# Kernel optimization log

Measured on AMD Instinct MI355X. Metric: run time of the kernel, lower is better.

## Reference

```python
import jax, jax.numpy as jnp
import numpy as np

EPS_BN = 1e-5
EPS_RENORM = 1e-9

def conv_bn_relu(x, W, g, b, m, v):
    # x: [B, Cin, N], W: [Cout, Cin] (1x1 conv, no bias). Eval-mode BN.
    y = jnp.einsum('oi,bin->bon', W, x)
    scale = (g / jnp.sqrt(v + EPS_BN))[None, :, None]
    bias = (b - m * g / jnp.sqrt(v + EPS_BN))[None, :, None]
    return jax.nn.relu(y * scale + bias)

def _make_params(key, cout, cin):
    k1, k2, k3, k4 = jax.random.split(key, 4)
    W = jax.random.normal(k1, (cout, cin), jnp.float32) * (1.0 / np.sqrt(cin))
    g = jax.random.uniform(k2, (cout,), jnp.float32, 0.5, 1.5)
    b = jax.random.normal(k3, (cout,), jnp.float32) * 0.1
    m = jax.random.normal(k4, (cout,), jnp.float32) * 0.1
    v = jax.random.uniform(jax.random.fold_in(key, 7), (cout,), jnp.float32, 0.5, 1.5)
    return W, g, b, m, v

def setup_inputs() -> dict:
    key = jax.random.key(0)
    ks = jax.random.split(key, 6)
    B, C, N = 8, 1024, 2048
    x = jax.random.normal(ks[0], (B, C, N), jnp.float32)
    inp = {'x': x}
    dims = [(1024, 1024), (1024, 1024), (128, 1024), (128, 1024), (1024, 1024)]
    for i, (co, ci) in enumerate(dims):
        W, g, b, m, v = _make_params(ks[i + 1], co, ci)
        inp[f'W{i+1}'] = W
        inp[f'g{i+1}'] = g
        inp[f'b{i+1}'] = b
        inp[f'm{i+1}'] = m
        inp[f'v{i+1}'] = v
    return inp

def reference(x,
              W1, g1, b1, m1, v1,
              W2, g2, b2, m2, v2,
              W3, g3, b3, m3, v3,
              W4, g4, b4, m4, v4,
              W5, g5, b5, m5, v5):
    x1 = conv_bn_relu(x, W1, g1, b1, m1, v1)          # [B,1024,N]
    v_ = conv_bn_relu(x1, W2, g2, b2, m2, v2)         # [B,1024,N]
    q_ = conv_bn_relu(x1, W3, g3, b3, m3, v3)         # [B,128,N]
    k_ = conv_bn_relu(x1, W4, g4, b4, m4, v4)         # [B,128,N]
    # q transposed: [B,N,128] @ [B,128,N] -> [B,N,N]
    scores = jnp.einsum('bcn,bcm->bnm', q_, k_)
    scores = jax.nn.softmax(scores, axis=-1)
    scores = scores / (EPS_RENORM + scores.sum(axis=1, keepdims=True))
    attn = jnp.einsum('bcn,bnm->bcm', v_, scores)     # [B,1024,N]
    x2 = conv_bn_relu(x1 - attn, W5, g5, b5, m5, v5)
    return x1 + x2
```

## Files before the change

### kernel.cpp

```cpp
#include <hip/hip_runtime.h>

typedef unsigned short u16;
using bf16x8 = __attribute__((ext_vector_type(8))) short;
using f32x4  = __attribute__((ext_vector_type(4))) float;

#define CH   1024
#define NP   2048
#define CQ   128

__device__ __forceinline__ float bf2f(u16 u){
  union { unsigned u; float f; } c; c.u = ((unsigned)u) << 16; return c.f;
}
__device__ __forceinline__ u16 f2bf(float f){
  unsigned x = __float_as_uint(f);
  unsigned r = (x + 0x7fffu + ((x >> 16) & 1u)) >> 16;
  return (u16)r;
}

__device__ __forceinline__ void gl2lds16(const u16* g, u16* l){
  __builtin_amdgcn_global_load_lds(
      (const __attribute__((address_space(1))) unsigned int*)(const void*)g,
      (__attribute__((address_space(3))) unsigned int*)(void*)l,
      16, 0, 0);
}

__global__ void ws_marker(float* out, float have_mb){
  out[0] = 1048576.0f + have_mb;
}

__global__ __launch_bounds__(256) void transpose_split(const float* __restrict__ x,
                                                       u16* __restrict__ xh,
                                                       u16* __restrict__ xl){
  const int bb = blockIdx.z;
  const int n0 = blockIdx.x * 64, c0 = blockIdx.y * 64;
  __shared__ float tile[64][65];
  const int t = threadIdx.x;
  const float* xb = x + ((size_t)bb*CH + c0)*NP + n0;
#pragma unroll
  for (int rr = 0; rr < 4; ++rr){
    const int c_l = (t >> 4) + rr*16;
    const int n_l = (t & 15) * 4;
    float4 v = *(const float4*)&xb[(size_t)c_l*NP + n_l];
    tile[c_l][n_l+0] = v.x; tile[c_l][n_l+1] = v.y;
    tile[c_l][n_l+2] = v.z; tile[c_l][n_l+3] = v.w;
  }
  __syncthreads();
  u16* oh = xh + ((size_t)bb*NP + n0)*CH + c0;
  u16* ol = xl + ((size_t)bb*NP + n0)*CH + c0;
#pragma unroll
  for (int rr = 0; rr < 4; ++rr){
    const int n_l = (t >> 4) + rr*16;
    const int c_l = (t & 15) * 4;
    ushort4 h, l;
    float v0 = tile[c_l+0][n_l], v1 = tile[c_l+1][n_l];
    float v2 = tile[c_l+2][n_l], v3 = tile[c_l+3][n_l];
    h.x = f2bf(v0); l.x = f2bf(v0 - bf2f(h.x));
    h.y = f2bf(v1); l.y = f2bf(v1 - bf2f(h.y));
    h.z = f2bf(v2); l.z = f2bf(v2 - bf2f(h.z));
    h.w = f2bf(v3); l.w = f2bf(v3 - bf2f(h.w));
    *(ushort4*)&oh[(size_t)n_l*CH + c_l] = h;
    *(ushort4*)&ol[(size_t)n_l*CH + c_l] = l;
  }
}

__global__ __launch_bounds__(256) void prep_all(
    const float* __restrict__ w0, const float* __restrict__ w1,
    const float* __restrict__ w2, const float* __restrict__ w3,
    const float* __restrict__ w4,
    u16* w1h, u16* w1l, u16* w2h,
    u16* w34h, u16* w34l, u16* w5h,
    const float* g3, const float* b3, const float* m3, const float* v3,
    const float* g4, const float* b4, const float* m4, const float* v4,
    float* p34, float* colsum){
  const int seg = blockIdx.y;
  if (seg == 5){
    for (int i = blockIdx.x*blockDim.x + threadIdx.x; i < 1024; i += gridDim.x*blockDim.x){
      const int grp = i >> 8, j = i & 255;
      const float* pa = (grp==0) ? g3 : (grp==1) ? b3 : (grp==2) ? m3 : v3;
      const float* pb = (grp==0) ? g4 : (grp==1) ? b4 : (grp==2) ? m4 : v4;
      p34[i] = (j < 128) ? pa[j] : pb[j-128];
    }
    return;
  }
  if (seg == 6){
    for (int i = blockIdx.x*blockDim.x + threadIdx.x; i < 8*NP; i += gridDim.x*blockDim.x)
      colsum[i] = 0.f;
    return;
  }
  const float* w; u16 *wh, *wl; int n;
  switch (seg){
    case 0:  w = w0; wh = w1h;           wl = w1l;           n = CH*CH; break;
    case 1:  w = w1; wh = w2h;           wl = nullptr;       n = CH*CH; break;
    case 2:  w = w2; wh = w34h;          wl = w34l;          n = CQ*CH; break;
    case 3:  w = w3; wh = w34h + CQ*CH;  wl = w34l + CQ*CH;  n = CQ*CH; break;
    default: w = w4; wh = w5h;           wl = nullptr;       n = CH*CH; break;
  }
  for (int i = blockIdx.x*blockDim.x + threadIdx.x; i < n; i += gridDim.x*blockDim.x){
    float v = w[i];
    u16 h = f2bf(v);
    wh[i] = h;
    if (wl) wl[i] = f2bf(v - bf2f(h));
  }
}

template<int EPI>
__global__ __launch_bounds__(256, 4) void gemm_plain(
    const u16* __restrict__ A, const u16* __restrict__ B,
    int lda, int ldb, long astr, long bstr, int K,
    void* __restrict__ out0, long ostr, int ldo,
    const float* __restrict__ pg, const float* __restrict__ pb,
    const float* __restrict__ pm, const float* __restrict__ pv,
    const u16* __restrict__ x1h, const u16* __restrict__ x1l,
    const float* __restrict__ cinv, const u16* __restrict__ cbf)
{
  __shared__ __align__(16) u16 sA[8192], sB[8192];
  const int tid  = threadIdx.x;
  const int lane = tid & 63, wave = tid >> 6;
  const int wr = wave & 1, wc = wave >> 1;
  const int l15 = lane & 15, q = lane >> 4;
  const int id = blockIdx.x;
  const int bb = id & 7;
  const int rest = id >> 3;
  const int by = rest & 7;
  const int bx = rest >> 3;
  const u16* Ab = A + (size_t)bb*astr + (size_t)bx*128*lda;
  const u16* Bb = B + (size_t)bb*bstr + (size_t)by*128*ldb;

  f32x4 acc[4][4] = {};
  f32x4 accR[4] = {};

  const int srow = tid >> 3;
  const int schunk = tid & 7;

  for (int kt = 0; kt < K; kt += 64){
#pragma unroll
    for (int r = 0; r < 4; ++r){
      const int row = r*32 + srow;
      const int gc8 = ((schunk ^ (row & 7)) << 3);
      gl2lds16(Ab + (size_t)row*lda + kt + gc8, &sA[r*2048 + tid*8]);
      gl2lds16(Bb + (size_t)row*ldb + kt + gc8, &sB[r*2048 + tid*8]);
    }
    __syncthreads();
#pragma unroll
    for (int s = 0; s < 2; ++s){
      bf16x8 af[4], bfr[4];
#pragma unroll
      for (int i = 0; i < 4; ++i){
        const int ra = wr*64 + i*16 + l15;
        af[i]  = *(const bf16x8*)&sA[ra*64 + (((s*4 + q) ^ (ra & 7)) << 3)];
        const int rb = wc*64 + i*16 + l15;
        bfr[i] = *(const bf16x8*)&sB[rb*64 + (((s*4 + q) ^ (rb & 7)) << 3)];
      }
      if constexpr (EPI == 1){
        const bf16x8 bcs = *(const bf16x8*)&cbf[(size_t)bb*NP + kt + s*32 + q*8];
#pragma unroll
        for (int i = 0; i < 4; ++i)
          accR[i] = __builtin_amdgcn_mfma_f32_16x16x32_bf16(af[i], bcs, accR[i], 0, 0, 0);
      }
#pragma unroll
      for (int i = 0; i < 4; ++i)
#pragma unroll
        for (int j = 0; j < 4; ++j)
          acc[i][j] = __builtin_amdgcn_mfma_f32_16x16x32_bf16(af[i], bfr[j], acc[i][j], 0, 0, 0);
    }
    __syncthreads();
  }

  const int rbase = bx*128 + wr*64;
  const int cbase = by*128 + wc*64;
#pragma unroll
  for (int j = 0; j < 4; ++j){
    const int gc = cbase + j*16 + l15;
    float scale = 0.f, bias = 0.f;
    if (EPI == 0 || EPI == 2){
      scale = pg[gc] * rsqrtf(pv[gc] + 1e-5f);
      bias  = pb[gc] - pm[gc]*scale;
    }
#pragma unroll
    for (int i = 0; i < 4; ++i){
      const int gr0 = rbase + i*16 + q*4;
      if (EPI == 0){
        const float4 cv = *(const float4*)&cinv[(size_t)bb*NP + gr0];
        ushort4 pk;
        pk.x = f2bf(fmaxf(acc[i][j][0]*scale + bias, 0.f) * cv.x);
        pk.y = f2bf(fmaxf(acc[i][j][1]*scale + bias, 0.f) * cv.y);
        pk.z = f2bf(fmaxf(acc[i][j][2]*scale + bias, 0.f) * cv.z);
        pk.w = f2bf(fmaxf(acc[i][j][3]*scale + bias, 0.f) * cv.w);
        *(ushort4*)&((u16*)out0)[(size_t)bb*ostr + (size_t)gc*ldo + gr0] = pk;
      } else if (EPI == 1){
#pragma unroll
        for (int r = 0; r < 4; ++r){
          const int gr = gr0 + r;
          const size_t idx = (size_t)bb*ostr + (size_t)gr*ldo + gc;
          const float rsv = 1.f / (1e-9f + accR[i][r]);
          const float x1v = bf2f(x1h[idx]) + bf2f(x1l[idx]);
          ((u16*)out0)[idx] = f2bf(x1v - acc[i][j][r]*rsv);
        }
      } else {
        float4 o4;
#pragma unroll
        for (int r = 0; r < 4; ++r){
          const int gr = gr0 + r;
          const size_t xidx = (size_t)bb*((size_t)NP*CH) + (size_t)gr*CH + gc;
          const float x2  = fmaxf(acc[i][j][r]*scale + bias, 0.f);
          const float x1v = bf2f(x1h[xidx]) + bf2f(x1l[xidx]);
          (&o4.x)[r] = x1v + x2;
        }
        *(float4*)&((float*)out0)[(size_t)bb*ostr + (size_t)gc*ldo + gr0] = o4;
      }
    }
  }
}

template<int EPI>
__global__ __launch_bounds__(256, 4) void gemm_split3(
    const u16* __restrict__ Ah, const u16* __restrict__ Al,
    const u16* __restrict__ Bh, const u16* __restrict__ Bl,
    int lda, int ldb, long astr, long bstr, int K,
    u16* __restrict__ outH, u16* __restrict__ outL,
    long ostr, int ldo,
    const float* __restrict__ pg, const float* __restrict__ pb,
    const float* __restrict__ pm, const float* __restrict__ pv,
    float* __restrict__ colsum, int gymask, int gyshift)
{
  __shared__ __align__(16) u16 sAh[4096], sAl[4096], sBh[4096], sBl[4096];
  const int tid  = threadIdx.x;
  const int lane = tid & 63, wave = tid >> 6;
  const int wr = wave & 1, wc = wave >> 1;
  const int l15 = lane & 15, q = lane >> 4;
  const int id = blockIdx.x;
  const int bb = id & 7;
  const int rest = id >> 3;
  const int by = rest & gymask;
  const int bx = rest >> gyshift;
  const u16* Abh = Ah + (size_t)bb*astr + (size_t)bx*128*lda;
  const u16* Abl = Al + (size_t)bb*astr + (size_t)bx*128*lda;
  const u16* Bbh = Bh + (size_t)bb*bstr + (size_t)by*128*ldb;
  const u16* Bbl = Bl + (size_t)bb*bstr + (size_t)by*128*ldb;

  f32x4 acc[4][4] = {};

  const int r0 = tid >> 2, r1 = r0 + 64;
  const int cs = (((tid & 3) ^ ((r0 >> 1) & 3)) << 3);

  int offA[4], offB[4];
#pragma unroll
  for (int i = 0; i < 4; ++i){
    const int ra = wr*64 + i*16 + l15;
    offA[i] = ra*32 + ((q ^ ((ra >> 1) & 3)) << 3);
    const int rb = wc*64 + i*16 + l15;
    offB[i] = rb*32 + ((q ^ ((rb >> 1) & 3)) << 3);
  }

  for (int kt = 0; kt < K; kt += 32){
    gl2lds16(Abh + (size_t)r0*lda + kt + cs, &sAh[tid*8]);
    gl2lds16(Abh + (size_t)r1*lda + kt + cs, &sAh[2048 + tid*8]);
    gl2lds16(Abl + (size_t)r0*lda + kt + cs, &sAl[tid*8]);
    gl2lds16(Abl + (size_t)r1*lda + kt + cs, &sAl[2048 + tid*8]);
    gl2lds16(Bbh + (size_t)r0*ldb + kt + cs, &sBh[tid*8]);
    gl2lds16(Bbh + (size_t)r1*ldb + kt + cs, &sBh[2048 + tid*8]);
    gl2lds16(Bbl + (size_t)r0*ldb + kt + cs, &sBl[tid*8]);
    gl2lds16(Bbl + (size_t)r1*ldb + kt + cs, &sBl[2048 + tid*8]);
    __syncthreads();
    bf16x8 ah[4], al[4], bh2[4], bl2[4];
#pragma unroll
    for (int i = 0; i < 4; ++i){
      ah[i] = *(const bf16x8*)&sAh[offA[i]];
      al[i] = *(const bf16x8*)&sAl[offA[i]];
    }
#pragma unroll
    for (int j = 0; j < 4; ++j){
      bh2[j] = *(const bf16x8*)&sBh[offB[j]];
      bl2[j] = *(const bf16x8*)&sBl[offB[j]];
    }
#pragma unroll
    for (int i = 0; i < 4; ++i)
#pragma unroll
      for (int j = 0; j < 4; ++j){
        acc[i][j] = __builtin_amdgcn_mfma_f32_16x16x32_bf16(ah[i], bh2[j], acc[i][j], 0, 0, 0);
        acc[i][j] = __builtin_amdgcn_mfma_f32_16x16x32_bf16(ah[i], bl2[j], acc[i][j], 0, 0, 0);
        acc[i][j] = __builtin_amdgcn_mfma_f32_16x16x32_bf16(al[i], bh2[j], acc[i][j], 0, 0, 0);
      }
    __syncthreads();
  }

  const int rbase = bx*128 + wr*64;
  const int cbase = by*128 + wc*64;

  if constexpr (EPI == 1){
    __shared__ float colpart[128];
    if (tid < 128) colpart[tid] = 0.f;
    __syncthreads();
#pragma unroll
    for (int j = 0; j < 4; ++j){
      const int gc = cbase + j*16 + l15;
      float lsum = 0.f;
#pragma unroll
      for (int i = 0; i < 4; ++i){
        const int gr0 = rbase + i*16 + q*4;
#pragma unroll
        for (int r = 0; r < 4; ++r){
          const float e = __expf(fminf(acc[i][j][r], 85.f));
          outH[(size_t)bb*ostr + (size_t)(gr0 + r)*ldo + gc] = f2bf(e);
          lsum += e;
        }
      }
      atomicAdd(&colpart[wc*64 + j*16 + l15], lsum);
    }
    __syncthreads();
    if (tid < 128) atomicAdd(&colsum[(size_t)bb*NP + (size_t)by*128 + tid], colpart[tid]);
  } else {
#pragma unroll
    for (int j = 0; j < 4; ++j){
      const int gc = cbase + j*16 + l15;
      const float scale = pg[gc] * rsqrtf(pv[gc] + 1e-5f);
      const float bias  = pb[gc] - pm[gc]*scale;
#pragma unroll
      for (int i = 0; i < 4; ++i){
        const int gr0 = rbase + i*16 + q*4;
#pragma unroll
        for (int r = 0; r < 4; ++r){
          const size_t idx = (size_t)bb*ostr + (size_t)(gr0 + r)*ldo + gc;
          const float y = fmaxf(acc[i][j][r]*scale + bias, 0.f);
          const u16 h = f2bf(y);
          outH[idx] = h;
          outL[idx] = f2bf(y - bf2f(h));
        }
      }
    }
  }
}

__global__ __launch_bounds__(256) void colinv_k(const float* __restrict__ cs,
                                                float* __restrict__ ci,
                                                u16* __restrict__ cib, int n){
  const int i = blockIdx.x*blockDim.x + threadIdx.x;
  if (i < n){
    const float v = 1.0f / cs[i];
    ci[i]  = v;
    cib[i] = f2bf(v);
  }
}

extern "C" void kernel_launch(void* const* d_in, const int* in_sizes, int n_in,
                              void* d_out, int out_size, void* d_ws, size_t ws_size,
                              hipStream_t stream){
  const float* x = (const float*)d_in[0];
  const float *W[5], *g[5], *bt[5], *mu[5], *vr[5];
  for (int i = 0; i < 5; ++i){
    W[i]  = (const float*)d_in[1 + 5*i + 0];
    g[i]  = (const float*)d_in[1 + 5*i + 1];
    bt[i] = (const float*)d_in[1 + 5*i + 2];
    mu[i] = (const float*)d_in[1 + 5*i + 3];
    vr[i] = (const float*)d_in[1 + 5*i + 4];
  }

  char* wp = (char*)d_ws;
  size_t off = 0;
  auto take = [&](size_t bytes) -> void* {
    void* p = wp + off;
    off = (off + bytes + 255) & ~(size_t)255;
    return p;
  };
  u16*   xh   = (u16*)take(33554432);
  u16*   xl   = (u16*)take(33554432);
  u16*   x1h  = (u16*)take(33554432);
  u16*   x1l  = (u16*)take(33554432);
  u16*   qkh  = (u16*)take(8388608);
  u16*   qkl  = (u16*)take(8388608);
  float* csum = (float*)take(65536);
  float* cinv = (float*)take(65536);
  u16*   cibf = (u16*)take(32768);
  u16*   w1h  = (u16*)take(2097152);
  u16*   w1l  = (u16*)take(2097152);
  u16*   w2h  = (u16*)take(2097152);
  u16*   w34h = (u16*)take(524288);
  u16*   w34l = (u16*)take(524288);
  u16*   w5h  = (u16*)take(2097152);
  float* p34  = (float*)take(4096);

  if (ws_size < off){
    ws_marker<<<1, 1, 0, stream>>>((float*)d_out, (float)(ws_size >> 20));
    return;
  }

  u16* vh   = xh;
  u16* tt   = xl;
  u16* expS = (u16*)d_out;

  prep_all<<<dim3(256, 7), 256, 0, stream>>>(
      W[0], W[1], W[2], W[3], W[4],
      w1h, w1l, w2h, w34h, w34l, w5h,
      g[2], bt[2], mu[2], vr[2], g[3], bt[3], mu[3], vr[3],
      p34, csum);

  transpose_split<<<dim3(32,16,8), 256, 0, stream>>>(x, xh, xl);

  gemm_split3<0><<<dim3(1024), 256, 0, stream>>>(
      xh, xl, w1h, w1l, CH, CH, (long)NP*CH, 0, CH,
      x1h, x1l, (long)NP*CH, CH, g[0], bt[0], mu[0], vr[0], nullptr, 7, 3);

  gemm_split3<0><<<dim3(256), 256, 0, stream>>>(
      x1h, x1l, w34h, w34l, CH, CH, (long)NP*CH, 0, CH,
      qkh, qkl, (long)NP*256, 256, p34, p34+256, p34+512, p34+768, nullptr, 1, 1);

  gemm_split3<1><<<dim3(2048), 256, 0, stream>>>(
      qkh + 128, qkl + 128, qkh, qkl, 256, 256, (long)NP*256, (long)NP*256, CQ,
      expS, nullptr, (long)NP*NP, NP,
      nullptr, nullptr, nullptr, nullptr, csum, 15, 4);

  colinv_k<<<dim3(64), 256, 0, stream>>>(csum, cinv, cibf, 8*NP);

  gemm_plain<0><<<dim3(1024), 256, 0, stream>>>(
      x1h, w2h, CH, CH, (long)NP*CH, 0, CH,
      vh, (long)CH*NP, NP, g[1], bt[1], mu[1], vr[1],
      nullptr, nullptr, cinv, nullptr);

  gemm_plain<1><<<dim3(1024), 256, 0, stream>>>(
      expS, vh, NP, NP, (long)NP*NP, (long)CH*NP, NP,
      tt, (long)NP*CH, CH, nullptr, nullptr, nullptr, nullptr,
      x1h, x1l, nullptr, cibf);

  gemm_plain<2><<<dim3(1024), 256, 0, stream>>>(
      tt, w5h, CH, CH, (long)NP*CH, 0, CH,
      d_out, (long)CH*NP, NP, g[4], bt[4], mu[4], vr[4],
      x1h, x1l, nullptr, nullptr);
}
```

Measured before the change: 645.4 us.

## Replace plain GEMM with 256x256-tile, 4-stage async-pipelined deep GEMM

The bf16 GEMM kernel used for the V projection, the attention-times-V product and the final conv now uses 512-thread blocks. Each block computes a 256x256 output tile with a K-step of 32 and a 4-deep ring of LDS buffers. Loads go directly from global memory to LDS three stages ahead, gated by explicit vmcnt waits and a single barrier per step, so loads overlap with MFMA work. For the attention GEMM, the column-inverse vector is cached in LDS. The cost is a large LDS footprint (about 132KB), more accumulator registers, and only 256 blocks, which may leave some of the mi355x's 256 CUs underfilled or limit occupancy to one block per CU.

```diff
diff --git a/kernel.cpp b/kernel.cpp
--- a/kernel.cpp
+++ b/kernel.cpp
@@ -104,7 +104,7 @@
 }
 
 template<int EPI>
-__global__ __launch_bounds__(256, 4) void gemm_plain(
+__global__ __launch_bounds__(512, 2) void gemm_deep(
     const u16* __restrict__ A, const u16* __restrict__ B,
     int lda, int ldb, long astr, long bstr, int K,
     void* __restrict__ out0, long ostr, int ldo,
@@ -113,61 +113,99 @@
     const u16* __restrict__ x1h, const u16* __restrict__ x1l,
     const float* __restrict__ cinv, const u16* __restrict__ cbf)
 {
-  __shared__ __align__(16) u16 sA[8192], sB[8192];
+  __shared__ __align__(16) u16 sA[4*8192];
+  __shared__ __align__(16) u16 sB[4*8192];
+  __shared__ __align__(16) u16 cl[2048];
+
   const int tid  = threadIdx.x;
-  const int lane = tid & 63, wave = tid >> 6;
-  const int wr = wave & 1, wc = wave >> 1;
+  const int lane = tid & 63;
+  const int wave = tid >> 6;
+  const int wr = wave >> 2, wc = wave & 3;
   const int l15 = lane & 15, q = lane >> 4;
   const int id = blockIdx.x;
   const int bb = id & 7;
   const int rest = id >> 3;
-  const int by = rest & 7;
-  const int bx = rest >> 3;
-  const u16* Ab = A + (size_t)bb*astr + (size_t)bx*128*lda;
-  const u16* Bb = B + (size_t)bb*bstr + (size_t)by*128*ldb;
-
-  f32x4 acc[4][4] = {};
-  f32x4 accR[4] = {};
-
-  const int srow = tid >> 3;
-  const int schunk = tid & 7;
-
-  for (int kt = 0; kt < K; kt += 64){
-#pragma unroll
-    for (int r = 0; r < 4; ++r){
-      const int row = r*32 + srow;
-      const int gc8 = ((schunk ^ (row & 7)) << 3);
-      gl2lds16(Ab + (size_t)row*lda + kt + gc8, &sA[r*2048 + tid*8]);
-      gl2lds16(Bb + (size_t)row*ldb + kt + gc8, &sB[r*2048 + tid*8]);
-    }
+  const int by = rest & 3;
+  const int bx = rest >> 2;
+
+  const u16* Ab = A + (size_t)bb*astr + (size_t)bx*256*lda;
+  const u16* Bb = B + (size_t)bb*bstr + (size_t)by*256*ldb;
+
+  const int srow = tid >> 2;
+  const int schunk = tid & 3;
+  const int cA = ((schunk ^ ((srow >> 1) & 3)) << 3);
+
+  auto stage = [&](int t){
+    const int buf = (t & 3) << 13;
+    const int kt = t << 5;
+    gl2lds16(Ab + (size_t)srow*lda + kt + cA,           &sA[buf + tid*8]);
+    gl2lds16(Ab + (size_t)(srow + 128)*lda + kt + cA,   &sA[buf + 4096 + tid*8]);
+    gl2lds16(Bb + (size_t)srow*ldb + kt + cA,           &sB[buf + tid*8]);
+    gl2lds16(Bb + (size_t)(srow + 128)*ldb + kt + cA,   &sB[buf + 4096 + tid*8]);
+  };
+
+  int offA[8], offB[4];
+#pragma unroll
+  for (int i = 0; i < 8; ++i){
+    const int ra = wr*128 + i*16 + l15;
+    offA[i] = ra*32 + ((q ^ ((ra >> 1) & 3)) << 3);
+  }
+#pragma unroll
+  for (int j = 0; j < 4; ++j){
+    const int rb = wc*64 + j*16 + l15;
+    offB[j] = rb*32 + ((q ^ ((rb >> 1) & 3)) << 3);
+  }
+
+  if constexpr (EPI == 1){
+    if (tid < 256)
+      *(bf16x8*)&cl[tid*8] = *(const bf16x8*)&cbf[(size_t)bb*NP + tid*8];
     __syncthreads();
-#pragma unroll
-    for (int s = 0; s < 2; ++s){
-      bf16x8 af[4], bfr[4];
-#pragma unroll
-      for (int i = 0; i < 4; ++i){
-        const int ra = wr*64 + i*16 + l15;
-        af[i]  = *(const bf16x8*)&sA[ra*64 + (((s*4 + q) ^ (ra & 7)) << 3)];
-        const int rb = wc*64 + i*16 + l15;
-        bfr[i] = *(const bf16x8*)&sB[rb*64 + (((s*4 + q) ^ (rb & 7)) << 3)];
-      }
-      if constexpr (EPI == 1){
-        const bf16x8 bcs = *(const bf16x8*)&cbf[(size_t)bb*NP + kt + s*32 + q*8];
-#pragma unroll
-        for (int i = 0; i < 4; ++i)
-          accR[i] = __builtin_amdgcn_mfma_f32_16x16x32_bf16(af[i], bcs, accR[i], 0, 0, 0);
-      }
-#pragma unroll
-      for (int i = 0; i < 4; ++i)
+  }
+
+  f32x4 acc[8][4] = {};
+  f32x4 accR[8] = {};
+
+  const int NT = K >> 5;
+  stage(0);
+  if (NT > 1) stage(1);
+  if (NT > 2) stage(2);
+
+  for (int t = 0; t < NT; ++t){
+    if (t < NT - 2)       asm volatile("s_waitcnt vmcnt(8)" ::: "memory");
+    else if (t == NT - 2) asm volatile("s_waitcnt vmcnt(4)" ::: "memory");
+    else                  asm volatile("s_waitcnt vmcnt(0)" ::: "memory");
+    __builtin_amdgcn_s_barrier();
+    asm volatile("" ::: "memory");
+    if (t + 3 < NT) stage(t + 3);
+
+    const int buf = (t & 3) << 13;
+    bf16x8 bv[4];
+#pragma unroll
+    for (int j = 0; j < 4; ++j) bv[j] = *(const bf16x8*)&sB[buf + offB[j]];
+
+    if constexpr (EPI == 1){
+      const bf16x8 cbs = *(const bf16x8*)&cl[(t << 5) + q*8];
+#pragma unroll
+      for (int i = 0; i < 8; ++i){
+        const bf16x8 a = *(const bf16x8*)&sA[buf + offA[i]];
+        accR[i] = __builtin_amdgcn_mfma_f32_16x16x32_bf16(a, cbs, accR[i], 0, 0, 0);
 #pragma unroll
         for (int j = 0; j < 4; ++j)
-          acc[i][j] = __builtin_amdgcn_mfma_f32_16x16x32_bf16(af[i], bfr[j], acc[i][j], 0, 0, 0);
-    }
-    __syncthreads();
-  }
-
-  const int rbase = bx*128 + wr*64;
-  const int cbase = by*128 + wc*64;
+          acc[i][j] = __builtin_amdgcn_mfma_f32_16x16x32_bf16(a, bv[j], acc[i][j], 0, 0, 0);
+      }
+    } else {
+#pragma unroll
+      for (int i = 0; i < 8; ++i){
+        const bf16x8 a = *(const bf16x8*)&sA[buf + offA[i]];
+#pragma unroll
+        for (int j = 0; j < 4; ++j)
+          acc[i][j] = __builtin_amdgcn_mfma_f32_16x16x32_bf16(a, bv[j], acc[i][j], 0, 0, 0);
+      }
+    }
+  }
+
+  const int rbase = bx*256 + wr*128;
+  const int cbase = by*256 + wc*64;
 #pragma unroll
   for (int j = 0; j < 4; ++j){
     const int gc = cbase + j*16 + l15;
@@ -177,7 +215,7 @@
       bias  = pb[gc] - pm[gc]*scale;
     }
 #pragma unroll
-    for (int i = 0; i < 4; ++i){
+    for (int i = 0; i < 8; ++i){
       const int gr0 = rbase + i*16 + q*4;
       if (EPI == 0){
         const float4 cv = *(const float4*)&cinv[(size_t)bb*NP + gr0];
@@ -411,17 +449,17 @@
 
   colinv_k<<<dim3(64), 256, 0, stream>>>(csum, cinv, cibf, 8*NP);
 
-  gemm_plain<0><<<dim3(1024), 256, 0, stream>>>(
+  gemm_deep<0><<<dim3(256), 512, 0, stream>>>(
       x1h, w2h, CH, CH, (long)NP*CH, 0, CH,
       vh, (long)CH*NP, NP, g[1], bt[1], mu[1], vr[1],
       nullptr, nullptr, cinv, nullptr);
 
-  gemm_plain<1><<<dim3(1024), 256, 0, stream>>>(
+  gemm_deep<1><<<dim3(256), 512, 0, stream>>>(
       expS, vh, NP, NP, (long)NP*NP, (long)CH*NP, NP,
       tt, (long)NP*CH, CH, nullptr, nullptr, nullptr, nullptr,
       x1h, x1l, nullptr, cibf);
 
-  gemm_plain<2><<<dim3(1024), 256, 0, stream>>>(
+  gemm_deep<2><<<dim3(256), 512, 0, stream>>>(
       tt, w5h, CH, CH, (long)NP*CH, 0, CH,
       d_out, (long)CH*NP, NP, g[4], bt[4], mu[4], vr[4],
       x1h, x1l, nullptr, nullptr);
```

Result: slower. 707.1 us (+9.6%).

## Replace plain bf16 GEMMs with 256x256-tile 8-wave ping-pong pipelined kernel

Applied to the files above, without the earlier changes.

Rewrites the three single-precision-input GEMMs (V projection, attention apply, final conv) into a 512-thread kernel with 256x256 output tiles. It double-buffers LDS and issues async global-to-LDS loads for the next K-step interleaved across four MFMA phases, using s_setprio and explicit barriers. The goal is to hide global latency and cut redundant A/B reloads through larger tiles. The cost is larger LDS use (about 132KB), lower occupancy, and a grid of only 256 blocks, which may underfill the CUs.

```diff
diff --git a/kernel.cpp b/kernel.cpp
--- a/kernel.cpp
+++ b/kernel.cpp
@@ -104,7 +104,7 @@
 }
 
 template<int EPI>
-__global__ __launch_bounds__(256, 4) void gemm_plain(
+__global__ __launch_bounds__(512, 2) void gemm_8p(
     const u16* __restrict__ A, const u16* __restrict__ B,
     int lda, int ldb, long astr, long bstr, int K,
     void* __restrict__ out0, long ostr, int ldo,
@@ -113,63 +113,152 @@
     const u16* __restrict__ x1h, const u16* __restrict__ x1l,
     const float* __restrict__ cinv, const u16* __restrict__ cbf)
 {
-  __shared__ __align__(16) u16 sA[8192], sB[8192];
+  __shared__ __align__(16) u16 sA[4*8192];
+  __shared__ __align__(16) u16 sB[4*8192];
+  __shared__ __align__(16) u16 cl[2048];
+
   const int tid  = threadIdx.x;
-  const int lane = tid & 63, wave = tid >> 6;
-  const int wr = wave & 1, wc = wave >> 1;
+  const int lane = tid & 63;
+  const int wave = tid >> 6;
+  const int wr = wave >> 1, wc = wave & 1;
   const int l15 = lane & 15, q = lane >> 4;
   const int id = blockIdx.x;
   const int bb = id & 7;
   const int rest = id >> 3;
-  const int by = rest & 7;
-  const int bx = rest >> 3;
-  const u16* Ab = A + (size_t)bb*astr + (size_t)bx*128*lda;
-  const u16* Bb = B + (size_t)bb*bstr + (size_t)by*128*ldb;
-
-  f32x4 acc[4][4] = {};
+  const int by = rest & 3;
+  const int bx = rest >> 2;
+
+  const u16* Ab = A + (size_t)bb*astr + (size_t)bx*256*lda;
+  const u16* Bb = B + (size_t)bb*bstr + (size_t)by*256*ldb;
+
+  const int sr0 = tid >> 3;
+  const int sg  = ((tid & 7) ^ (sr0 & 7)) << 3;
+
+  auto stageA = [&](int half, int V){
+    u16* dst = &sA[((((V & 1) << 1) + half) << 13)];
+    const u16* src = Ab + (size_t)(half*128 + sr0)*lda + V*64 + sg;
+    gl2lds16(src, dst + tid*8);
+    gl2lds16(src + (size_t)64*lda, dst + 4096 + tid*8);
+  };
+  auto stageB = [&](int half, int V){
+    u16* dst = &sB[((((V & 1) << 1) + half) << 13)];
+    const u16* src = Bb + (size_t)(half*128 + sr0)*ldb + V*64 + sg;
+    gl2lds16(src, dst + tid*8);
+    gl2lds16(src + (size_t)64*ldb, dst + 4096 + tid*8);
+  };
+
+  const int ckx = l15 & 7;
+  const int ck0 = ((0 + q) ^ ckx) << 3;
+  const int ck1 = ((4 + q) ^ ckx) << 3;
+  int rpA[4], rpB[8];
+#pragma unroll
+  for (int i = 0; i < 4; ++i) rpA[i] = (((wr & 1) << 6) + i*16 + l15) << 6;
+#pragma unroll
+  for (int j = 0; j < 8; ++j) rpB[j] = (j*16 + l15) << 6;
+  const int aHalf = (wr >> 1) << 13;
+  const int bHalf = wc << 13;
+
+  if constexpr (EPI == 1){
+    if (tid < 256)
+      *(bf16x8*)&cl[tid*8] = *(const bf16x8*)&cbf[(size_t)bb*NP + tid*8];
+  }
+  __syncthreads();
+
+  f32x4 acc[4][8] = {};
   f32x4 accR[4] = {};
 
-  const int srow = tid >> 3;
-  const int schunk = tid & 7;
-
-  for (int kt = 0; kt < K; kt += 64){
-#pragma unroll
-    for (int r = 0; r < 4; ++r){
-      const int row = r*32 + srow;
-      const int gc8 = ((schunk ^ (row & 7)) << 3);
-      gl2lds16(Ab + (size_t)row*lda + kt + gc8, &sA[r*2048 + tid*8]);
-      gl2lds16(Bb + (size_t)row*ldb + kt + gc8, &sB[r*2048 + tid*8]);
-    }
-    __syncthreads();
-#pragma unroll
-    for (int s = 0; s < 2; ++s){
-      bf16x8 af[4], bfr[4];
-#pragma unroll
-      for (int i = 0; i < 4; ++i){
-        const int ra = wr*64 + i*16 + l15;
-        af[i]  = *(const bf16x8*)&sA[ra*64 + (((s*4 + q) ^ (ra & 7)) << 3)];
-        const int rb = wc*64 + i*16 + l15;
-        bfr[i] = *(const bf16x8*)&sB[rb*64 + (((s*4 + q) ^ (rb & 7)) << 3)];
-      }
-      if constexpr (EPI == 1){
-        const bf16x8 bcs = *(const bf16x8*)&cbf[(size_t)bb*NP + kt + s*32 + q*8];
-#pragma unroll
-        for (int i = 0; i < 4; ++i)
-          accR[i] = __builtin_amdgcn_mfma_f32_16x16x32_bf16(af[i], bcs, accR[i], 0, 0, 0);
-      }
+  const int NT = K >> 6;
+  stageA(0, 0); stageA(1, 0); stageB(0, 0); stageB(1, 0);
+  if (NT > 1) stageA(0, 1);
+
+  for (int U = 0; U < NT; ++U){
+    const int aB = ((U & 1) << 14) + aHalf;
+    const int bB = ((U & 1) << 14) + bHalf;
+    bf16x8 af[4], bfr[4], cbs;
+
+    if (U + 1 < NT) stageA(1, U + 1);
+    if (U < NT - 1) asm volatile("s_waitcnt vmcnt(4)" ::: "memory");
+    else            asm volatile("s_waitcnt vmcnt(0)" ::: "memory");
+    __builtin_amdgcn_s_barrier();
+#pragma unroll
+    for (int i = 0; i < 4; ++i) af[i]  = *(const bf16x8*)&sA[aB + rpA[i] + ck0];
+#pragma unroll
+    for (int j = 0; j < 4; ++j) bfr[j] = *(const bf16x8*)&sB[bB + rpB[j] + ck0];
+    if constexpr (EPI == 1) cbs = *(const bf16x8*)&cl[U*64 + q*8];
+    asm volatile("s_waitcnt lgkmcnt(0)" ::: "memory");
+    __builtin_amdgcn_sched_barrier(0);
+    __builtin_amdgcn_s_setprio(1);
+    if constexpr (EPI == 1){
 #pragma unroll
       for (int i = 0; i < 4; ++i)
-#pragma unroll
-        for (int j = 0; j < 4; ++j)
-          acc[i][j] = __builtin_amdgcn_mfma_f32_16x16x32_bf16(af[i], bfr[j], acc[i][j], 0, 0, 0);
-    }
-    __syncthreads();
-  }
-
-  const int rbase = bx*128 + wr*64;
-  const int cbase = by*128 + wc*64;
-#pragma unroll
-  for (int j = 0; j < 4; ++j){
+        accR[i] = __builtin_amdgcn_mfma_f32_16x16x32_bf16(af[i], cbs, accR[i], 0, 0, 0);
+    }
+#pragma unroll
+    for (int i = 0; i < 4; ++i)
+#pragma unroll
+      for (int j = 0; j < 4; ++j)
+        acc[i][j] = __builtin_amdgcn_mfma_f32_16x16x32_bf16(af[i], bfr[j], acc[i][j], 0, 0, 0);
+    __builtin_amdgcn_s_setprio(0);
+    __builtin_amdgcn_s_barrier();
+
+#pragma unroll
+    for (int j = 0; j < 4; ++j) bfr[j] = *(const bf16x8*)&sB[bB + rpB[4+j] + ck0];
+    if (U + 1 < NT) stageB(0, U + 1);
+    __builtin_amdgcn_s_barrier();
+    asm volatile("s_waitcnt lgkmcnt(0)" ::: "memory");
+    __builtin_amdgcn_sched_barrier(0);
+    __builtin_amdgcn_s_setprio(1);
+#pragma unroll
+    for (int i = 0; i < 4; ++i)
+#pragma unroll
+      for (int j = 0; j < 4; ++j)
+        acc[i][4+j] = __builtin_amdgcn_mfma_f32_16x16x32_bf16(af[i], bfr[j], acc[i][4+j], 0, 0, 0);
+    __builtin_amdgcn_s_setprio(0);
+    __builtin_amdgcn_s_barrier();
+
+#pragma unroll
+    for (int i = 0; i < 4; ++i) af[i]  = *(const bf16x8*)&sA[aB + rpA[i] + ck1];
+#pragma unroll
+    for (int j = 0; j < 4; ++j) bfr[j] = *(const bf16x8*)&sB[bB + rpB[j] + ck1];
+    if constexpr (EPI == 1) cbs = *(const bf16x8*)&cl[U*64 + 32 + q*8];
+    if (U + 1 < NT) stageB(1, U + 1);
+    __builtin_amdgcn_s_barrier();
+    asm volatile("s_waitcnt lgkmcnt(0)" ::: "memory");
+    __builtin_amdgcn_sched_barrier(0);
+    __builtin_amdgcn_s_setprio(1);
+    if constexpr (EPI == 1){
+#pragma unroll
+      for (int i = 0; i < 4; ++i)
+        accR[i] = __builtin_amdgcn_mfma_f32_16x16x32_bf16(af[i], cbs, accR[i], 0, 0, 0);
+    }
+#pragma unroll
+    for (int i = 0; i < 4; ++i)
+#pragma unroll
+      for (int j = 0; j < 4; ++j)
+        acc[i][j] = __builtin_amdgcn_mfma_f32_16x16x32_bf16(af[i], bfr[j], acc[i][j], 0, 0, 0);
+    __builtin_amdgcn_s_setprio(0);
+    __builtin_amdgcn_s_barrier();
+
+#pragma unroll
+    for (int j = 0; j < 4; ++j) bfr[j] = *(const bf16x8*)&sB[bB + rpB[4+j] + ck1];
+    if (U + 2 < NT) stageA(0, U + 2);
+    __builtin_amdgcn_s_barrier();
+    asm volatile("s_waitcnt lgkmcnt(0)" ::: "memory");
+    __builtin_amdgcn_sched_barrier(0);
+    __builtin_amdgcn_s_setprio(1);
+#pragma unroll
+    for (int i = 0; i < 4; ++i)
+#pragma unroll
+      for (int j = 0; j < 4; ++j)
+        acc[i][4+j] = __builtin_amdgcn_mfma_f32_16x16x32_bf16(af[i], bfr[j], acc[i][4+j], 0, 0, 0);
+    __builtin_amdgcn_s_setprio(0);
+    __builtin_amdgcn_s_barrier();
+  }
+
+  const int rbase = bx*256 + wr*64;
+  const int cbase = by*256 + wc*128;
+#pragma unroll
+  for (int j = 0; j < 8; ++j){
     const int gc = cbase + j*16 + l15;
     float scale = 0.f, bias = 0.f;
     if (EPI == 0 || EPI == 2){
@@ -411,17 +500,17 @@
 
   colinv_k<<<dim3(64), 256, 0, stream>>>(csum, cinv, cibf, 8*NP);
 
-  gemm_plain<0><<<dim3(1024), 256, 0, stream>>>(
+  gemm_8p<0><<<dim3(256), 512, 0, stream>>>(
       x1h, w2h, CH, CH, (long)NP*CH, 0, CH,
       vh, (long)CH*NP, NP, g[1], bt[1], mu[1], vr[1],
       nullptr, nullptr, cinv, nullptr);
 
-  gemm_plain<1><<<dim3(1024), 256, 0, stream>>>(
+  gemm_8p<1><<<dim3(256), 512, 0, stream>>>(
       expS, vh, NP, NP, (long)NP*NP, (long)CH*NP, NP,
       tt, (long)NP*CH, CH, nullptr, nullptr, nullptr, nullptr,
       x1h, x1l, nullptr, cibf);
 
-  gemm_plain<2><<<dim3(1024), 256, 0, stream>>>(
+  gemm_8p<2><<<dim3(256), 512, 0, stream>>>(
       tt, w5h, CH, CH, (long)NP*CH, 0, CH,
       d_out, (long)CH*NP, NP, g[4], bt[4], mu[4], vr[4],
       x1h, x1l, nullptr, nullptr);
```

Measured after the change: 628.8 us. 2.6% less time.

## Enlarge GEMM tiles to 256x256 with 512 threads and double-buffered LDS prefetch

Applied to the files above, without the earlier changes.

The plain bf16 GEMMs (V projection, attention apply and final conv) and the first split-precision conv GEMM move to 256x256 output tiles. Each uses 8 waves per block and a grid of 256 blocks. The next K-slice is loaded into a second LDS buffer while the current one is multiplied, and the column-scale vector for the attention GEMM is cached in LDS. This aims to cut global/LDS traffic per FLOP and hide load latency. In exchange it uses about 128KB of LDS per block, adds register pressure from 32 accumulators per wave, and runs at low occupancy with one block per CU.

```diff
diff --git a/kernel.cpp b/kernel.cpp
--- a/kernel.cpp
+++ b/kernel.cpp
@@ -104,7 +104,7 @@
 }
 
 template<int EPI>
-__global__ __launch_bounds__(256, 4) void gemm_plain(
+__global__ __launch_bounds__(512, 2) void gemm_2ph(
     const u16* __restrict__ A, const u16* __restrict__ B,
     int lda, int ldb, long astr, long bstr, int K,
     void* __restrict__ out0, long ostr, int ldo,
@@ -113,63 +113,99 @@
     const u16* __restrict__ x1h, const u16* __restrict__ x1l,
     const float* __restrict__ cinv, const u16* __restrict__ cbf)
 {
-  __shared__ __align__(16) u16 sA[8192], sB[8192];
+  __shared__ __align__(16) u16 sA[2][16384];
+  __shared__ __align__(16) u16 sB[2][16384];
+  __shared__ __align__(16) u16 cl[2048];
+
   const int tid  = threadIdx.x;
-  const int lane = tid & 63, wave = tid >> 6;
-  const int wr = wave & 1, wc = wave >> 1;
+  const int lane = tid & 63;
+  const int wave = tid >> 6;
+  const int wr = wave >> 1, wc = wave & 1;
   const int l15 = lane & 15, q = lane >> 4;
   const int id = blockIdx.x;
   const int bb = id & 7;
   const int rest = id >> 3;
-  const int by = rest & 7;
-  const int bx = rest >> 3;
-  const u16* Ab = A + (size_t)bb*astr + (size_t)bx*128*lda;
-  const u16* Bb = B + (size_t)bb*bstr + (size_t)by*128*ldb;
-
-  f32x4 acc[4][4] = {};
+  const int by = rest & 3;
+  const int bx = rest >> 2;
+
+  const u16* Ab = A + (size_t)bb*astr + (size_t)bx*256*lda;
+  const u16* Bb = B + (size_t)bb*bstr + (size_t)by*256*ldb;
+
+  const int sr0 = tid >> 3;
+  const int sg  = (((tid & 7) ^ (sr0 & 7)) << 3);
+
+  auto stage = [&](int kt, int bsel){
+    u16* dA = sA[bsel]; u16* dB = sB[bsel];
+#pragma unroll
+    for (int rr = 0; rr < 4; ++rr){
+      gl2lds16(Ab + (size_t)(rr*64 + sr0)*lda + kt + sg, dA + rr*4096 + tid*8);
+      gl2lds16(Bb + (size_t)(rr*64 + sr0)*ldb + kt + sg, dB + rr*4096 + tid*8);
+    }
+  };
+
+  int rpA[4], rpB[8];
+#pragma unroll
+  for (int i = 0; i < 4; ++i) rpA[i] = (wr*64 + i*16 + l15) << 6;
+#pragma unroll
+  for (int j = 0; j < 8; ++j) rpB[j] = (wc*128 + j*16 + l15) << 6;
+  const int ckx = l15 & 7;
+  const int ck0 = ((0 + q) ^ ckx) << 3;
+  const int ck1 = ((4 + q) ^ ckx) << 3;
+
+  if constexpr (EPI == 1){
+    if (tid < 256)
+      *(bf16x8*)&cl[tid*8] = *(const bf16x8*)&cbf[(size_t)bb*NP + tid*8];
+  }
+
+  f32x4 acc[4][8] = {};
   f32x4 accR[4] = {};
 
-  const int srow = tid >> 3;
-  const int schunk = tid & 7;
-
-  for (int kt = 0; kt < K; kt += 64){
-#pragma unroll
-    for (int r = 0; r < 4; ++r){
-      const int row = r*32 + srow;
-      const int gc8 = ((schunk ^ (row & 7)) << 3);
-      gl2lds16(Ab + (size_t)row*lda + kt + gc8, &sA[r*2048 + tid*8]);
-      gl2lds16(Bb + (size_t)row*ldb + kt + gc8, &sB[r*2048 + tid*8]);
-    }
+  const int NT = K >> 6;
+  stage(0, 0);
+  __syncthreads();
+
+  for (int t = 0; t < NT; ++t){
+    if (t + 1 < NT) stage((t + 1) << 6, (t + 1) & 1);
+    const u16* cA = sA[t & 1];
+    const u16* cB = sB[t & 1];
+    bf16x8 af[4], bfr[8];
+#pragma unroll
+    for (int i = 0; i < 4; ++i) af[i]  = *(const bf16x8*)&cA[rpA[i] + ck0];
+#pragma unroll
+    for (int j = 0; j < 8; ++j) bfr[j] = *(const bf16x8*)&cB[rpB[j] + ck0];
+    if constexpr (EPI == 1){
+      const bf16x8 cbs = *(const bf16x8*)&cl[(t << 6) + q*8];
+#pragma unroll
+      for (int i = 0; i < 4; ++i)
+        accR[i] = __builtin_amdgcn_mfma_f32_16x16x32_bf16(af[i], cbs, accR[i], 0, 0, 0);
+    }
+#pragma unroll
+    for (int i = 0; i < 4; ++i)
+#pragma unroll
+      for (int j = 0; j < 8; ++j)
+        acc[i][j] = __builtin_amdgcn_mfma_f32_16x16x32_bf16(af[i], bfr[j], acc[i][j], 0, 0, 0);
+#pragma unroll
+    for (int i = 0; i < 4; ++i) af[i]  = *(const bf16x8*)&cA[rpA[i] + ck1];
+#pragma unroll
+    for (int j = 0; j < 8; ++j) bfr[j] = *(const bf16x8*)&cB[rpB[j] + ck1];
+    if constexpr (EPI == 1){
+      const bf16x8 cbs = *(const bf16x8*)&cl[(t << 6) + 32 + q*8];
+#pragma unroll
+      for (int i = 0; i < 4; ++i)
+        accR[i] = __builtin_amdgcn_mfma_f32_16x16x32_bf16(af[i], cbs, accR[i], 0, 0, 0);
+    }
+#pragma unroll
+    for (int i = 0; i < 4; ++i)
+#pragma unroll
+      for (int j = 0; j < 8; ++j)
+        acc[i][j] = __builtin_amdgcn_mfma_f32_16x16x32_bf16(af[i], bfr[j], acc[i][j], 0, 0, 0);
     __syncthreads();
-#pragma unroll
-    for (int s = 0; s < 2; ++s){
-      bf16x8 af[4], bfr[4];
-#pragma unroll
-      for (int i = 0; i < 4; ++i){
-        const int ra = wr*64 + i*16 + l15;
-        af[i]  = *(const bf16x8*)&sA[ra*64 + (((s*4 + q) ^ (ra & 7)) << 3)];
-        const int rb = wc*64 + i*16 + l15;
-        bfr[i] = *(const bf16x8*)&sB[rb*64 + (((s*4 + q) ^ (rb & 7)) << 3)];
-      }
-      if constexpr (EPI == 1){
-        const bf16x8 bcs = *(const bf16x8*)&cbf[(size_t)bb*NP + kt + s*32 + q*8];
-#pragma unroll
-        for (int i = 0; i < 4; ++i)
-          accR[i] = __builtin_amdgcn_mfma_f32_16x16x32_bf16(af[i], bcs, accR[i], 0, 0, 0);
-      }
-#pragma unroll
-      for (int i = 0; i < 4; ++i)
-#pragma unroll
-        for (int j = 0; j < 4; ++j)
-          acc[i][j] = __builtin_amdgcn_mfma_f32_16x16x32_bf16(af[i], bfr[j], acc[i][j], 0, 0, 0);
-    }
-    __syncthreads();
-  }
-
-  const int rbase = bx*128 + wr*64;
-  const int cbase = by*128 + wc*64;
-#pragma unroll
-  for (int j = 0; j < 4; ++j){
+  }
+
+  const int rbase = bx*256 + wr*64;
+  const int cbase = by*256 + wc*128;
+#pragma unroll
+  for (int j = 0; j < 8; ++j){
     const int gc = cbase + j*16 + l15;
     float scale = 0.f, bias = 0.f;
     if (EPI == 0 || EPI == 2){
@@ -207,6 +243,117 @@
           (&o4.x)[r] = x1v + x2;
         }
         *(float4*)&((float*)out0)[(size_t)bb*ostr + (size_t)gc*ldo + gr0] = o4;
+      }
+    }
+  }
+}
+
+__global__ __launch_bounds__(512, 2) void gemm_split_big(
+    const u16* __restrict__ Ah, const u16* __restrict__ Al,
+    const u16* __restrict__ Bh, const u16* __restrict__ Bl,
+    int lda, int ldb, long astr, long bstr, int K,
+    u16* __restrict__ outH, u16* __restrict__ outL,
+    long ostr, int ldo,
+    const float* __restrict__ pg, const float* __restrict__ pb,
+    const float* __restrict__ pm, const float* __restrict__ pv)
+{
+  __shared__ __align__(16) u16 sAh[2][8192], sAl[2][8192];
+  __shared__ __align__(16) u16 sBh[2][8192], sBl[2][8192];
+
+  const int tid  = threadIdx.x;
+  const int lane = tid & 63;
+  const int wave = tid >> 6;
+  const int wr = wave >> 1, wc = wave & 1;
+  const int l15 = lane & 15, q = lane >> 4;
+  const int id = blockIdx.x;
+  const int bb = id & 7;
+  const int rest = id >> 3;
+  const int by = rest & 3;
+  const int bx = rest >> 2;
+
+  const u16* Abh = Ah + (size_t)bb*astr + (size_t)bx*256*lda;
+  const u16* Abl = Al + (size_t)bb*astr + (size_t)bx*256*lda;
+  const u16* Bbh = Bh + (size_t)bb*bstr + (size_t)by*256*ldb;
+  const u16* Bbl = Bl + (size_t)bb*bstr + (size_t)by*256*ldb;
+
+  const int sr = tid >> 2;
+  const int sg = (((tid & 3) ^ ((sr >> 1) & 3)) << 3);
+
+  auto stage = [&](int kt, int bsel){
+    gl2lds16(Abh + (size_t)sr*lda        + kt + sg, &sAh[bsel][tid*8]);
+    gl2lds16(Abh + (size_t)(sr+128)*lda  + kt + sg, &sAh[bsel][4096 + tid*8]);
+    gl2lds16(Abl + (size_t)sr*lda        + kt + sg, &sAl[bsel][tid*8]);
+    gl2lds16(Abl + (size_t)(sr+128)*lda  + kt + sg, &sAl[bsel][4096 + tid*8]);
+    gl2lds16(Bbh + (size_t)sr*ldb        + kt + sg, &sBh[bsel][tid*8]);
+    gl2lds16(Bbh + (size_t)(sr+128)*ldb  + kt + sg, &sBh[bsel][4096 + tid*8]);
+    gl2lds16(Bbl + (size_t)sr*ldb        + kt + sg, &sBl[bsel][tid*8]);
+    gl2lds16(Bbl + (size_t)(sr+128)*ldb  + kt + sg, &sBl[bsel][4096 + tid*8]);
+  };
+
+  int offA[4], offB[8];
+#pragma unroll
+  for (int i = 0; i < 4; ++i){
+    const int ra = wr*64 + i*16 + l15;
+    offA[i] = ra*32 + ((q ^ ((ra >> 1) & 3)) << 3);
+  }
+#pragma unroll
+  for (int j = 0; j < 8; ++j){
+    const int rb = wc*128 + j*16 + l15;
+    offB[j] = rb*32 + ((q ^ ((rb >> 1) & 3)) << 3);
+  }
+
+  f32x4 acc[4][8] = {};
+
+  const int NT = K >> 5;
+  stage(0, 0);
+  __syncthreads();
+
+  for (int t = 0; t < NT; ++t){
+    if (t + 1 < NT) stage((t + 1) << 5, (t + 1) & 1);
+    const int cur = t & 1;
+    bf16x8 ah[4], al2[4];
+#pragma unroll
+    for (int i = 0; i < 4; ++i){
+      ah[i]  = *(const bf16x8*)&sAh[cur][offA[i]];
+      al2[i] = *(const bf16x8*)&sAl[cur][offA[i]];
+    }
+#pragma unroll
+    for (int jh = 0; jh < 2; ++jh){
+      bf16x8 bh[4], bl[4];
+#pragma unroll
+      for (int j = 0; j < 4; ++j){
+        bh[j] = *(const bf16x8*)&sBh[cur][offB[jh*4 + j]];
+        bl[j] = *(const bf16x8*)&sBl[cur][offB[jh*4 + j]];
+      }
+#pragma unroll
+      for (int i = 0; i < 4; ++i)
+#pragma unroll
+        for (int j = 0; j < 4; ++j){
+          acc[i][jh*4+j] = __builtin_amdgcn_mfma_f32_16x16x32_bf16(ah[i],  bh[j], acc[i][jh*4+j], 0, 0, 0);
+          acc[i][jh*4+j] = __builtin_amdgcn_mfma_f32_16x16x32_bf16(ah[i],  bl[j], acc[i][jh*4+j], 0, 0, 0);
+          acc[i][jh*4+j] = __builtin_amdgcn_mfma_f32_16x16x32_bf16(al2[i], bh[j], acc[i][jh*4+j], 0, 0, 0);
+        }
+    }
+    __syncthreads();
+  }
+
+  const int rbase = bx*256 + wr*64;
+  const int cbase = by*256 + wc*128;
+#pragma unroll
+  for (int j = 0; j < 8; ++j){
+    const int gc = cbase + j*16 + l15;
+    const float scale = pg[gc] * rsqrtf(pv[gc] + 1e-5f);
+    const float bias  = pb[gc] - pm[gc]*scale;
+#pragma unroll
+    for (int i = 0; i < 4; ++i){
+      const int gr0 = rbase + i*16 + q*4;
+#pragma unroll
+      for (int r = 0; r < 4; ++r){
+        const size_t idx = (size_t)bb*ostr + (size_t)(gr0 + r)*ldo + gc;
+        const float y = fmaxf(acc[i][j][r]*scale + bias, 0.f);
+        const u16 h = f2bf(y);
+        outH[idx] = h;
+        outL[idx] = f2bf(y - bf2f(h));
       }
     }
   }
@@ -396,9 +543,9 @@
 
   transpose_split<<<dim3(32,16,8), 256, 0, stream>>>(x, xh, xl);
 
-  gemm_split3<0><<<dim3(1024), 256, 0, stream>>>(
+  gemm_split_big<<<dim3(256), 512, 0, stream>>>(
       xh, xl, w1h, w1l, CH, CH, (long)NP*CH, 0, CH,
-      x1h, x1l, (long)NP*CH, CH, g[0], bt[0], mu[0], vr[0], nullptr, 7, 3);
+      x1h, x1l, (long)NP*CH, CH, g[0], bt[0], mu[0], vr[0]);
 
   gemm_split3<0><<<dim3(256), 256, 0, stream>>>(
       x1h, x1l, w34h, w34l, CH, CH, (long)NP*CH, 0, CH,
@@ -411,17 +558,17 @@
 
   colinv_k<<<dim3(64), 256, 0, stream>>>(csum, cinv, cibf, 8*NP);
 
-  gemm_plain<0><<<dim3(1024), 256, 0, stream>>>(
+  gemm_2ph<0><<<dim3(256), 512, 0, stream>>>(
       x1h, w2h, CH, CH, (long)NP*CH, 0, CH,
       vh, (long)CH*NP, NP, g[1], bt[1], mu[1], vr[1],
       nullptr, nullptr, cinv, nullptr);
 
-  gemm_plain<1><<<dim3(1024), 256, 0, stream>>>(
+  gemm_2ph<1><<<dim3(256), 512, 0, stream>>>(
       expS, vh, NP, NP, (long)NP*NP, (long)CH*NP, NP,
       tt, (long)NP*CH, CH, nullptr, nullptr, nullptr, nullptr,
       x1h, x1l, nullptr, cibf);
 
-  gemm_plain<2><<<dim3(1024), 256, 0, stream>>>(
+  gemm_2ph<2><<<dim3(256), 512, 0, stream>>>(
       tt, w5h, CH, CH, (long)NP*CH, 0, CH,
       d_out, (long)CH*NP, NP, g[4], bt[4], mu[4], vr[4],
       x1h, x1l, nullptr, nullptr);
```

Measured after the change: 599.1 us (median of 2 runs). 1.08x faster.
